# Kernel optimization log

Hardware: AMD Instinct MI355X
Metric: run time of the kernel (lower is better)

The kernel has to match this reference:

```python
import jax, jax.numpy as jnp
import numpy as np

B, S, D = 8, 2048, 256


def setup_inputs() -> dict:
    key = jax.random.key(0)
    ks = jax.random.split(key, 8)
    sc = 0.05
    return {
        "q": jax.random.normal(ks[0], (B, S, D), jnp.float32),
        "k": jax.random.normal(ks[1], (B, S, D), jnp.float32),
        "v": jax.random.normal(ks[2], (B, S, D), jnp.float32),
        "Wi0": jax.random.normal(ks[3], (D, D), jnp.float32) * sc,
        "Wi1": jax.random.normal(ks[4], (D, D), jnp.float32) * sc,
        "Wo0": jax.random.normal(ks[5], (D, D), jnp.float32) * sc,
        "Wo1": jax.random.normal(ks[6], (D, D), jnp.float32) * sc,
        "bo0": jnp.zeros((D,), jnp.float32),
        "bo1": jnp.zeros((D,), jnp.float32),
    }


def reference(q, k, v, Wi0, Wi1, Wo0, Wo1, bo0, bo1):
    d = q.shape[-1]
    scale = 1.0 / np.sqrt(d).astype(np.float32)
    # (B, S, S) shared score matrix
    scores = jnp.einsum("bqd,bkd->bqk", q, k) * scale
    s = scores.shape[-1]
    i = jnp.arange(s)[:, None]
    j = jnp.arange(s)[None, :]
    NEG = jnp.float32(-1e9)
    # fw: mask strictly-lower triangle (attend to j >= i); bw: mask strictly-upper (j <= i)
    fw_w = jax.nn.softmax(jnp.where(j < i, NEG, scores), axis=-1)
    bw_w = jax.nn.softmax(jnp.where(j > i, NEG, scores), axis=-1)
    fw_v = jnp.einsum("bqk,bkd->bqd", fw_w, v)
    bw_v = jnp.einsum("bqk,bkd->bqd", bw_w, v)
    # fusion gates: sigmoid(in_gate(v) + out_gate(att_v))  (torch Linear: x @ W.T + b)
    fw_gate = jax.nn.sigmoid(v @ Wi0.T + fw_v @ Wo0.T + bo0)
    bw_gate = jax.nn.sigmoid(v @ Wi1.T + bw_v @ Wo1.T + bo1)
    fw_out = fw_gate * fw_v + (1.0 - fw_gate) * v
    bw_out = bw_gate * bw_v + (1.0 - bw_gate) * v
    return jnp.concatenate((fw_out, bw_out), axis=-1)
```

## Files before the change

### kernel.cpp

```cpp
#include <hip/hip_runtime.h>
#include <stdint.h>


typedef unsigned short u16;
typedef unsigned int u32;
typedef __attribute__((ext_vector_type(8))) short short8;
typedef __attribute__((ext_vector_type(4))) float f32x4;

#define B_ 8
#define S_ 2048
#define D_ 256
#define QB 64
#define NP 32

#define LOG2E 1.44269504088896340736f
#define QSCALE (LOG2E/16.0f)

#define KSWZ_OFF 0
#define VT_OFF   (8u<<20)
#define VT_PERIOD 40960u
#define VT_BATCH (32u*VT_PERIOD)
#define WBF_OFF  (VT_OFF + 8u*VT_BATCH)

#define LDS_K  0
#define LDS_V  65536
#define LDS_P  147456

__device__ __forceinline__ u16 f2bf(float f) {
    union { float f; u32 u; } x; x.f = f;
    u32 u = x.u + 0x7fffu + ((x.u >> 16) & 1u);
    return (u16)(u >> 16);
}
__device__ __forceinline__ short8 pack8(float4 a, float4 b) {
    short8 r;
    r[0] = (short)f2bf(a.x); r[1] = (short)f2bf(a.y);
    r[2] = (short)f2bf(a.z); r[3] = (short)f2bf(a.w);
    r[4] = (short)f2bf(b.x); r[5] = (short)f2bf(b.y);
    r[6] = (short)f2bf(b.z); r[7] = (short)f2bf(b.w);
    return r;
}
__device__ __forceinline__ f32x4 mfma16(short8 a, short8 b, f32x4 c) {
    return __builtin_amdgcn_mfma_f32_16x16x32_bf16(a, b, c, 0, 0, 0);
}
__device__ __forceinline__ void gload_lds(const void* g, void* lds) {
    __builtin_amdgcn_global_load_lds(
        (const __attribute__((address_space(1))) void*)g,
        (__attribute__((address_space(3))) void*)lds, 16, 0, 0);
}

__global__ __launch_bounds__(256, 1)
void prep_kernel(const float* __restrict__ k, const float* __restrict__ v,
                 const float* __restrict__ w0, const float* __restrict__ w1,
                 const float* __restrict__ w2, const float* __restrict__ w3,
                 char* __restrict__ ws)
{
    const int tid = (int)threadIdx.x;
    const int bid = (int)blockIdx.x;

    if (bid < 512) {
        __shared__ float vs[32][257];
        const int b = bid >> 6, jt = bid & 63;
        const float* vb = v + ((size_t)b * S_ + (size_t)jt * 32) * D_;
        const int j = tid >> 3, d0 = (tid & 7) * 32;
        #pragma unroll
        for (int i = 0; i < 8; ++i) {
            float4 x = *(const float4*)(vb + (size_t)j * D_ + d0 + i * 4);
            vs[j][d0 + i * 4 + 0] = x.x; vs[j][d0 + i * 4 + 1] = x.y;
            vs[j][d0 + i * 4 + 2] = x.z; vs[j][d0 + i * 4 + 3] = x.w;
        }
        __syncthreads();
        char* ob = ws + VT_OFF + (size_t)b * VT_BATCH + (size_t)(jt >> 1) * VT_PERIOD
                   + (size_t)(jt & 1) * 20480 + (size_t)tid * 80;
        short8 o[4];
        #pragma unroll
        for (int jj = 0; jj < 32; ++jj) o[jj >> 3][jj & 7] = (short)f2bf(vs[jj][tid]);
        #pragma unroll
        for (int i = 0; i < 4; ++i) *(short8*)(ob + i * 16) = o[i];
    } else if (bid < 1024) {
        const int t = bid - 512, b = t >> 6, jt = t & 63;
        const float* kb = k + ((size_t)b * S_ + (size_t)jt * 32) * D_;
        char* ob = ws + KSWZ_OFF + (size_t)(b * 64 + jt) * 16384;
        #pragma unroll
        for (int it = 0; it < 4; ++it) {
            int gi = tid + it * 256;
            int r = gi >> 5, cg = gi & 31;
            float4 x0 = *(const float4*)(kb + (size_t)r * D_ + cg * 8);
            float4 x1 = *(const float4*)(kb + (size_t)r * D_ + cg * 8 + 4);
            *(short8*)(ob + r * 512 + ((cg * 16) ^ ((r & 7) << 4))) = pack8(x0, x1);
        }
    } else {
        const int t = bid - 1024, m = t >> 4, db = t & 15;
        const float* wsrc = (m == 0 ? w0 : m == 1 ? w1 : m == 2 ? w2 : w3)
                            + (size_t)(db * 16) * D_;
        char* ob = ws + WBF_OFF + (size_t)(db * 4 + m) * 8192;
        #pragma unroll
        for (int it = 0; it < 2; ++it) {
            int gi = tid + it * 256;
            int r = gi >> 5, cg = gi & 31;
            float4 x0 = *(const float4*)(wsrc + (size_t)r * D_ + cg * 8);
            float4 x1 = *(const float4*)(wsrc + (size_t)r * D_ + cg * 8 + 4);
            *(short8*)(ob + r * 512 + ((cg * 16) ^ ((r & 7) << 4))) = pack8(x0, x1);
        }
    }
}

#define PV_TAIL(accD, accS)                                                    \
    {                                                                          \
        short8 pa = *(const short8*)&pw[c * 40 + g * 8];                       \
        __builtin_amdgcn_s_setprio(1);                                         \
        accS = mfma16(pa, onesb, accS);                                        \
        _Pragma("unroll")                                                      \
        for (int db = 0; db < 16; ++db) {                                      \
            short8 vb = *(const short8*)(vcur + (db * 16 + c) * 80 + g * 16);  \
            accD[db] = mfma16(pa, vb, accD[db]);                               \
        }                                                                      \
        __builtin_amdgcn_s_setprio(0);                                         \
    }

#define DO_FULL(accD, accS)                                                    \
    {                                                                          \
        _Pragma("unroll")                                                      \
        for (int r = 0; r < 4; ++r) {                                          \
            pw[(g * 4 + r) * 40 + c]      = f2bf(exp2f(sc0[r]));               \
            pw[(g * 4 + r) * 40 + 16 + c] = f2bf(exp2f(sc1[r]));               \
        }                                                                      \
        PV_TAIL(accD, accS)                                                    \
    }

#define DO_MASK(CMPOP, accD, accS)                                             \
    {                                                                          \
        _Pragma("unroll")                                                      \
        for (int r = 0; r < 4; ++r) {                                          \
            int qq = r0 + g * 4 + r;                                           \
            float e0 = ((j0 + c) CMPOP qq) ? exp2f(sc0[r]) : 0.0f;             \
            float e1 = ((j0 + 16 + c) CMPOP qq) ? exp2f(sc1[r]) : 0.0f;        \
            pw[(g * 4 + r) * 40 + c]      = f2bf(e0);                          \
            pw[(g * 4 + r) * 40 + 16 + c] = f2bf(e1);                          \
        }                                                                      \
        PV_TAIL(accD, accS)                                                    \
    }

__global__ __launch_bounds__(512, 2)
void attn_kernel(const float* __restrict__ q, const char* __restrict__ kswz,
                 const char* __restrict__ vt, const char* __restrict__ wbf,
                 const float* __restrict__ v,
                 const float* __restrict__ bo0, const float* __restrict__ bo1,
                 float* __restrict__ out)
{
    __shared__ char smem[157696];
    u16* pl = (u16*)(smem + LDS_P);

    const int tid = (int)threadIdx.x;
    const int wv = tid >> 6, lane = tid & 63;
    const int h = wv >> 2, wl = wv & 3;
    const int g = lane >> 4, c = lane & 15;
    const int bid = (int)blockIdx.x;
    const int b = bid & 7, qi = bid >> 3;
    const int q0 = qi * QB;
    const int r0 = q0 + wl * 16;
    const int dt = r0 >> 5;
    u16* pw = pl + wv * 640;

    const char* kbaseg = kswz + (size_t)b * (64 * 16384);
    const char* vbaseg = vt + (size_t)b * VT_BATCH;

    short8 qf[8];
    {
        const float* qp = q + ((size_t)b * S_ + (size_t)(r0 + c)) * D_;
        #pragma unroll
        for (int ks = 0; ks < 8; ++ks) {
            float4 a = *(const float4*)(qp + ks * 32 + g * 8);
            float4 d = *(const float4*)(qp + ks * 32 + g * 8 + 4);
            a.x *= QSCALE; a.y *= QSCALE; a.z *= QSCALE; a.w *= QSCALE;
            d.x *= QSCALE; d.y *= QSCALE; d.z *= QSCALE; d.w *= QSCALE;
            qf[ks] = pack8(a, d);
        }
    }

    short8 onesb;
    #pragma unroll
    for (int i = 0; i < 8; ++i) onesb[i] = (c == 0) ? (short)0x3F80 : (short)0;

    const f32x4 zero4 = {0.f, 0.f, 0.f, 0.f};
    f32x4 accF[16], accB[16], accSF = zero4, accSB = zero4;
    #pragma unroll
    for (int i = 0; i < 16; ++i) { accF[i] = zero4; accB[i] = zero4; }

    #define STAGE(t, buf)                                                      \
        {                                                                      \
            const char* kg_ = kbaseg + (size_t)(t) * 32768;                    \
            const char* vg_ = vbaseg + (size_t)(t) * VT_PERIOD;                \
            _Pragma("unroll")                                                  \
            for (int i = 0; i < 4; ++i) {                                      \
                int off = i * 8192 + wv * 1024;                                \
                gload_lds(kg_ + off + lane * 16, smem + LDS_K + (buf) * 32768 + off); \
            }                                                                  \
            _Pragma("unroll")                                                  \
            for (int i = 0; i < 5; ++i) {                                      \
                int off = i * 8192 + wv * 1024;                                \
                gload_lds(vg_ + off + lane * 16, smem + LDS_V + (buf) * 40960 + off); \
            }                                                                  \
        }

    STAGE(0, 0);
    __syncthreads();

    const int swz = (c & 7) << 4;

    #pragma unroll 1
    for (int t = 0; t < NP; ++t) {
        const int cur = t & 1;
        if (t + 1 < NP) STAGE(t + 1, cur ^ 1);

        const int jw = 2 * t + h;
        const int j0 = jw * 32;
        const char* kcur = smem + LDS_K + cur * 32768 + h * 16384;
        const char* vcur = smem + LDS_V + cur * 40960 + h * 20480;

        f32x4 sc0 = zero4, sc1 = zero4;
        __builtin_amdgcn_s_setprio(1);
        #pragma unroll
        for (int ks = 0; ks < 8; ++ks) {
            int inner = (ks * 64 + g * 16) ^ swz;
            short8 kb0 = *(const short8*)(kcur + c * 512 + inner);
            short8 kb1 = *(const short8*)(kcur + (16 + c) * 512 + inner);
            sc0 = mfma16(qf[ks], kb0, sc0);
            sc1 = mfma16(qf[ks], kb1, sc1);
        }
        __builtin_amdgcn_s_setprio(0);

        if (jw < dt) {
            DO_FULL(accB, accSB)
        } else if (jw > dt) {
            DO_FULL(accF, accSF)
        } else {
            DO_MASK(<=, accB, accSB)
            DO_MASK(>=, accF, accSF)
        }
        __syncthreads();
    }

    float* sumsA = (float*)(smem + LDS_P);
    float* sumsB = (float*)(smem + LDS_P + 256);

    if (h == 1) {
        float* dst = (float*)smem + wl * 4096;
        #pragma unroll
        for (int db = 0; db < 16; ++db)
            #pragma unroll
            for (int r = 0; r < 4; ++r)
                dst[(g * 4 + r) * 256 + db * 16 + c] = accF[db][r];
        if (c == 0) {
            #pragma unroll
            for (int r = 0; r < 4; ++r) sumsA[wl * 16 + g * 4 + r] = accSF[r];
        }
    } else {
        float* dst = (float*)(smem + LDS_V) + wl * 4096;
        #pragma unroll
        for (int db = 0; db < 16; ++db)
            #pragma unroll
            for (int r = 0; r < 4; ++r)
                dst[(g * 4 + r) * 256 + db * 16 + c] = accB[db][r];
        if (c == 0) {
            #pragma unroll
            for (int r = 0; r < 4; ++r) sumsB[wl * 16 + g * 4 + r] = accSB[r];
        }
    }
    __syncthreads();

    f32x4 merged[16];
    if (h == 0) {
        const float* src = (const float*)smem + wl * 4096;
        float rs[4];
        #pragma unroll
        for (int r = 0; r < 4; ++r) {
            float so = __shfl(accSF[r], lane & 48);
            rs[r] = 1.0f / (so + sumsA[wl * 16 + g * 4 + r]);
        }
        #pragma unroll
        for (int db = 0; db < 16; ++db)
            #pragma unroll
            for (int r = 0; r < 4; ++r)
                merged[db][r] = (accF[db][r] + src[(g * 4 + r) * 256 + db * 16 + c]) * rs[r];
    } else {
        const float* src = (const float*)(smem + LDS_V) + wl * 4096;
        float rs[4];
        #pragma unroll
        for (int r = 0; r < 4; ++r) {
            float so = __shfl(accSB[r], lane & 48);
            rs[r] = 1.0f / (so + sumsB[wl * 16 + g * 4 + r]);
        }
        #pragma unroll
        for (int db = 0; db < 16; ++db)
            #pragma unroll
            for (int r = 0; r < 4; ++r)
                merged[db][r] = (accB[db][r] + src[(g * 4 + r) * 256 + db * 16 + c]) * rs[r];
    }
    __syncthreads();

    {
        char* imgb = smem + h * 32768;
        #pragma unroll
        for (int db = 0; db < 16; ++db)
            #pragma unroll
            for (int r = 0; r < 4; ++r) {
                int lr = wl * 16 + g * 4 + r;
                int cb = (db * 16 + c) * 2;
                *(u16*)(imgb + lr * 512 + (cb ^ ((lr & 7) << 4))) = f2bf(merged[db][r]);
            }
    }
    #define WSTAGE(db, buf)                                                    \
        {                                                                      \
            const char* gsrc = wbf + (size_t)(db) * 32768;                     \
            _Pragma("unroll")                                                  \
            for (int i = 0; i < 4; ++i) {                                      \
                int off = i * 8192 + wv * 1024;                                \
                gload_lds(gsrc + off + lane * 16,                              \
                          smem + LDS_V + (buf) * 32768 + off);                 \
            }                                                                  \
        }
    WSTAGE(0, 0);
    __syncthreads();

    short8 af[8], vf[8];
    {
        const char* imgb = smem + h * 32768;
        int lr = wl * 16 + c;
        #pragma unroll
        for (int ks = 0; ks < 8; ++ks) {
            int inner = (ks * 64 + g * 16) ^ swz;
            af[ks] = *(const short8*)(imgb + lr * 512 + inner);
        }
        const float* vp = v + ((size_t)b * S_ + (size_t)(r0 + c)) * D_;
        #pragma unroll
        for (int ks = 0; ks < 8; ++ks) {
            float4 a = *(const float4*)(vp + ks * 32 + g * 8);
            float4 d = *(const float4*)(vp + ks * 32 + g * 8 + 4);
            vf[ks] = pack8(a, d);
        }
    }

    const float* bias = (h == 0) ? bo0 : bo1;
    const float* vrow = v + ((size_t)b * S_ + (size_t)r0) * D_;
    float* ob = out + ((size_t)b * S_ + (size_t)r0) * 512 + h * 256;
    #pragma unroll
    for (int db = 0; db < 16; ++db) {
        const int cu2 = db & 1;
        if (db + 1 < 16) WSTAGE(db + 1, cu2 ^ 1);

        float bb = bias[db * 16 + c];
        f32x4 a = {bb, bb, bb, bb};
        const char* wc = smem + LDS_V + cu2 * 32768 + h * 16384;
        __builtin_amdgcn_s_setprio(1);
        #pragma unroll
        for (int ks = 0; ks < 8; ++ks) {
            int inner = (ks * 64 + g * 16) ^ swz;
            short8 wi = *(const short8*)(wc + c * 512 + inner);
            short8 wo = *(const short8*)(wc + 8192 + c * 512 + inner);
            a = mfma16(vf[ks], wi, a);
            a = mfma16(af[ks], wo, a);
        }
        __builtin_amdgcn_s_setprio(0);

        #pragma unroll
        for (int r = 0; r < 4; ++r) {
            int row = g * 4 + r;
            float vv = vrow[(size_t)row * D_ + db * 16 + c];
            float gate = 1.0f / (1.0f + exp2f(-a[r] * LOG2E));
            float m = merged[db][r];
            ob[(size_t)row * 512 + db * 16 + c] = gate * m + (1.0f - gate) * vv;
        }
        __syncthreads();
    }
}

extern "C" void kernel_launch(void* const* d_in, const int* in_sizes, int n_in,
                              void* d_out, int out_size, void* d_ws, size_t ws_size,
                              hipStream_t stream)
{
    const float* q   = (const float*)d_in[0];
    const float* k   = (const float*)d_in[1];
    const float* v   = (const float*)d_in[2];
    const float* Wi0 = (const float*)d_in[3];
    const float* Wi1 = (const float*)d_in[4];
    const float* Wo0 = (const float*)d_in[5];
    const float* Wo1 = (const float*)d_in[6];
    const float* bo0 = (const float*)d_in[7];
    const float* bo1 = (const float*)d_in[8];
    float* out = (float*)d_out;
    char* ws = (char*)d_ws;
    (void)in_sizes; (void)n_in; (void)ws_size; (void)out_size;

    prep_kernel<<<dim3(1088), dim3(256), 0, stream>>>(k, v, Wi0, Wo0, Wi1, Wo1, ws);
    attn_kernel<<<dim3(256), dim3(512), 0, stream>>>(q, ws + KSWZ_OFF, ws + VT_OFF,
                                                     ws + WBF_OFF, v, bo0, bo1, out);
}
```

Baseline: 103.4 us.

## Keep softmax probabilities in registers via transposed QK MFMA and 16x16x16 PV

Computes the score tile transposed (K as the A operand) so each lane already holds the probabilities in the A-operand layout of a 16x16x16 bf16 MFMA. P no longer round-trips through LDS, and packing uses v_cvt_pk_bf16_f32. The cost is twice as many PV MFMAs, each half as wide, plus split V reads. The freed LDS scratch shrinks shared memory, and the row sums are moved to a new offset.

```diff
diff --git a/kernel.cpp b/kernel.cpp
--- a/kernel.cpp
+++ b/kernel.cpp
@@ -5,6 +5,7 @@
 typedef unsigned short u16;
 typedef unsigned int u32;
 typedef __attribute__((ext_vector_type(8))) short short8;
+typedef __attribute__((ext_vector_type(4))) short short4v;
 typedef __attribute__((ext_vector_type(4))) float f32x4;
 
 #define B_ 8
@@ -24,7 +25,7 @@
 
 #define LDS_K  0
 #define LDS_V  65536
-#define LDS_P  147456
+#define LDS_SUM 131072
 
 __device__ __forceinline__ u16 f2bf(float f) {
     union { float f; u32 u; } x; x.f = f;
@@ -41,6 +42,24 @@
 }
 __device__ __forceinline__ f32x4 mfma16(short8 a, short8 b, f32x4 c) {
     return __builtin_amdgcn_mfma_f32_16x16x32_bf16(a, b, c, 0, 0, 0);
+}
+__device__ __forceinline__ f32x4 mfma161(short4v a, short4v b, f32x4 c) {
+#if __has_builtin(__builtin_amdgcn_mfma_f32_16x16x16bf16_1k)
+    return __builtin_amdgcn_mfma_f32_16x16x16bf16_1k(a, b, c, 0, 0, 0);
+#elif __has_builtin(__builtin_amdgcn_mfma_f32_16x16x16_bf16)
+    return __builtin_amdgcn_mfma_f32_16x16x16_bf16(a, b, c, 0, 0, 0);
+#else
+    f32x4 d;
+    asm volatile("v_mfma_f32_16x16x16_bf16 %0, %1, %2, %3"
+                 : "=v"(d) : "v"(a), "v"(b), "v"(c));
+    return d;
+#endif
+}
+__device__ __forceinline__ short4v pkbf(float a0, float a1, float a2, float a3) {
+    union { u32 w[2]; short4v v; } u;
+    asm("v_cvt_pk_bf16_f32 %0, %1, %2" : "=v"(u.w[0]) : "v"(a0), "v"(a1));
+    asm("v_cvt_pk_bf16_f32 %0, %1, %2" : "=v"(u.w[1]) : "v"(a2), "v"(a3));
+    return u.v;
 }
 __device__ __forceinline__ void gload_lds(const void* g, void* lds) {
     __builtin_amdgcn_global_load_lds(
@@ -104,40 +123,20 @@
     }
 }
 
-#define PV_TAIL(accD, accS)                                                    \
+#define PV_REG(paL_, paH_, accD, accS)                                         \
     {                                                                          \
-        short8 pa = *(const short8*)&pw[c * 40 + g * 8];                       \
         __builtin_amdgcn_s_setprio(1);                                         \
-        accS = mfma16(pa, onesb, accS);                                        \
+        accS = mfma161(paL_, onesb4, accS);                                    \
+        accS = mfma161(paH_, onesb4, accS);                                    \
         _Pragma("unroll")                                                      \
         for (int db = 0; db < 16; ++db) {                                      \
-            short8 vb = *(const short8*)(vcur + (db * 16 + c) * 80 + g * 16);  \
-            accD[db] = mfma16(pa, vb, accD[db]);                               \
+            const char* vp_ = vcur + (db * 16 + c) * 80 + g * 8;               \
+            short4v vlo = *(const short4v*)(vp_);                              \
+            short4v vhi = *(const short4v*)(vp_ + 32);                         \
+            accD[db] = mfma161(paL_, vlo, accD[db]);                           \
+            accD[db] = mfma161(paH_, vhi, accD[db]);                           \
         }                                                                      \
         __builtin_amdgcn_s_setprio(0);                                         \
-    }
-
-#define DO_FULL(accD, accS)                                                    \
-    {                                                                          \
-        _Pragma("unroll")                                                      \
-        for (int r = 0; r < 4; ++r) {                                          \
-            pw[(g * 4 + r) * 40 + c]      = f2bf(exp2f(sc0[r]));               \
-            pw[(g * 4 + r) * 40 + 16 + c] = f2bf(exp2f(sc1[r]));               \
-        }                                                                      \
-        PV_TAIL(accD, accS)                                                    \
-    }
-
-#define DO_MASK(CMPOP, accD, accS)                                             \
-    {                                                                          \
-        _Pragma("unroll")                                                      \
-        for (int r = 0; r < 4; ++r) {                                          \
-            int qq = r0 + g * 4 + r;                                           \
-            float e0 = ((j0 + c) CMPOP qq) ? exp2f(sc0[r]) : 0.0f;             \
-            float e1 = ((j0 + 16 + c) CMPOP qq) ? exp2f(sc1[r]) : 0.0f;        \
-            pw[(g * 4 + r) * 40 + c]      = f2bf(e0);                          \
-            pw[(g * 4 + r) * 40 + 16 + c] = f2bf(e1);                          \
-        }                                                                      \
-        PV_TAIL(accD, accS)                                                    \
     }
 
 __global__ __launch_bounds__(512, 2)
@@ -147,8 +146,7 @@
                  const float* __restrict__ bo0, const float* __restrict__ bo1,
                  float* __restrict__ out)
 {
-    __shared__ char smem[157696];
-    u16* pl = (u16*)(smem + LDS_P);
+    __shared__ char smem[147456];
 
     const int tid = (int)threadIdx.x;
     const int wv = tid >> 6, lane = tid & 63;
@@ -159,7 +157,6 @@
     const int q0 = qi * QB;
     const int r0 = q0 + wl * 16;
     const int dt = r0 >> 5;
-    u16* pw = pl + wv * 640;
 
     const char* kbaseg = kswz + (size_t)b * (64 * 16384);
     const char* vbaseg = vt + (size_t)b * VT_BATCH;
@@ -177,9 +174,9 @@
         }
     }
 
-    short8 onesb;
+    short4v onesb4;
     #pragma unroll
-    for (int i = 0; i < 8; ++i) onesb[i] = (c == 0) ? (short)0x3F80 : (short)0;
+    for (int i = 0; i < 4; ++i) onesb4[i] = (c == 0) ? (short)0x3F80 : (short)0;
 
     const f32x4 zero4 = {0.f, 0.f, 0.f, 0.f};
     f32x4 accF[16], accB[16], accSF = zero4, accSB = zero4;
@@ -217,31 +214,51 @@
         const char* kcur = smem + LDS_K + cur * 32768 + h * 16384;
         const char* vcur = smem + LDS_V + cur * 40960 + h * 20480;
 
-        f32x4 sc0 = zero4, sc1 = zero4;
+        f32x4 scT0 = zero4, scT1 = zero4;
         __builtin_amdgcn_s_setprio(1);
         #pragma unroll
         for (int ks = 0; ks < 8; ++ks) {
             int inner = (ks * 64 + g * 16) ^ swz;
             short8 kb0 = *(const short8*)(kcur + c * 512 + inner);
             short8 kb1 = *(const short8*)(kcur + (16 + c) * 512 + inner);
-            sc0 = mfma16(qf[ks], kb0, sc0);
-            sc1 = mfma16(qf[ks], kb1, sc1);
+            scT0 = mfma16(kb0, qf[ks], scT0);
+            scT1 = mfma16(kb1, qf[ks], scT1);
         }
         __builtin_amdgcn_s_setprio(0);
 
-        if (jw < dt) {
-            DO_FULL(accB, accSB)
-        } else if (jw > dt) {
-            DO_FULL(accF, accSF)
+        if (jw != dt) {
+            short4v paL = pkbf(exp2f(scT0[0]), exp2f(scT0[1]), exp2f(scT0[2]), exp2f(scT0[3]));
+            short4v paH = pkbf(exp2f(scT1[0]), exp2f(scT1[1]), exp2f(scT1[2]), exp2f(scT1[3]));
+            if (jw < dt) {
+                PV_REG(paL, paH, accB, accSB);
+            } else {
+                PV_REG(paL, paH, accF, accSF);
+            }
         } else {
-            DO_MASK(<=, accB, accSB)
-            DO_MASK(>=, accF, accSF)
+            const int qq = r0 + c;
+            float m0[4], m1[4], n0[4], n1[4];
+            #pragma unroll
+            for (int r = 0; r < 4; ++r) {
+                int jgl = j0 + 4 * g + r;
+                int jgh = j0 + 16 + 4 * g + r;
+                float v0 = exp2f(scT0[r]), v1 = exp2f(scT1[r]);
+                m0[r] = (jgl <= qq) ? v0 : 0.0f;
+                m1[r] = (jgh <= qq) ? v1 : 0.0f;
+                n0[r] = (jgl >= qq) ? v0 : 0.0f;
+                n1[r] = (jgh >= qq) ? v1 : 0.0f;
+            }
+            short4v pbL = pkbf(m0[0], m0[1], m0[2], m0[3]);
+            short4v pbH = pkbf(m1[0], m1[1], m1[2], m1[3]);
+            short4v pfL = pkbf(n0[0], n0[1], n0[2], n0[3]);
+            short4v pfH = pkbf(n1[0], n1[1], n1[2], n1[3]);
+            PV_REG(pbL, pbH, accB, accSB);
+            PV_REG(pfL, pfH, accF, accSF);
         }
         __syncthreads();
     }
 
-    float* sumsA = (float*)(smem + LDS_P);
-    float* sumsB = (float*)(smem + LDS_P + 256);
+    float* sumsA = (float*)(smem + LDS_SUM);
+    float* sumsB = (float*)(smem + LDS_SUM + 256);
 
     if (h == 1) {
         float* dst = (float*)smem + wl * 4096;
```

After: 111.0 us. +7.3%, slower.
